# Kernel optimization log

Measured on AMD Instinct MI355X. Metric: run time of the kernel, lower is better.

Reference implementation:

```python
import jax, jax.numpy as jnp
import numpy as np

D_MODEL, D_FF, N_EXPERTS, TOP_K = 1024, 2048, 8, 2
B, S = 2, 2048

def setup_inputs() -> dict:
    key = jax.random.key(0)
    k1, k2, k3, k4 = jax.random.split(key, 4)
    scale = 0.02
    return {
        "x": jax.random.normal(k1, (B, S, D_MODEL), dtype=jnp.float32),
        "gate_w": jax.random.normal(k2, (D_MODEL, N_EXPERTS), dtype=jnp.float32) * scale,
        "w1": jax.random.normal(k3, (N_EXPERTS, D_MODEL, D_FF), dtype=jnp.float32) * scale,
        "w2": jax.random.normal(k4, (N_EXPERTS, D_FF, D_MODEL), dtype=jnp.float32) * scale,
    }

def reference(x, gate_w, w1, w2):
    # --- Router (eval mode: no exploration noise, no dropout) ---
    router_logits = jnp.einsum('bsd,de->bse', x, gate_w)          # [B,S,E]
    top_logits, top_idx = jax.lax.top_k(router_logits, TOP_K)      # [B,S,K]
    top_w = jax.nn.softmax(top_logits, axis=-1)                    # [B,S,K]
    # topk indices are distinct per token, so per-(token,expert) combine weight
    # is the sum over k of weight_k * 1[idx_k == e] (matches torch gather/argmax logic)
    combine = jnp.sum(
        jax.nn.one_hot(top_idx, N_EXPERTS, dtype=x.dtype) * top_w[..., None],
        axis=-2)                                                   # [B,S,E]
    # --- Experts: dense-compute formulation of the gather/MLP/scatter loop ---
    h = jax.nn.silu(jnp.einsum('bsd,edf->ebsf', x, w1))            # [E,B,S,Dff]
    y = jnp.einsum('ebsf,efd->ebsd', h, w2)                        # [E,B,S,D]
    out = jnp.einsum('ebsd,bse->bsd', y, combine)                  # [B,S,D]
    return out
```

## Files before the change

kernel.cpp:

```cpp
#include <hip/hip_runtime.h>
#include <cstdint>
#include <cstddef>

#define D_MODEL 1024
#define D_FF    2048
#define N_EXP   8
#define NTOK    4096
#define NASSIGN (NTOK * 2)
#define MAXTILE 72

typedef __bf16 bf16_t;
typedef bf16_t bf16x8 __attribute__((ext_vector_type(8)));
typedef float  f32x4  __attribute__((ext_vector_type(4)));

typedef __attribute__((address_space(3))) void       lds_void;
typedef const __attribute__((address_space(1))) void gl_void;

__device__ __forceinline__ unsigned short f2b(float f) {
  union { float f; unsigned u; } v; v.f = f;
  unsigned u = v.u;
  unsigned r = (u + 0x7FFFu + ((u >> 16) & 1u)) >> 16;
  return (unsigned short)r;
}
__device__ __forceinline__ float b2f(unsigned short b) {
  union { unsigned u; float f; } v; v.u = ((unsigned)b) << 16; return v.f;
}

__device__ __forceinline__ void transpose_pair(
    const float* __restrict__ ein, unsigned short* __restrict__ eout,
    int R, int C, int c00, int r0, unsigned* T0, unsigned* T1, int tid)
{
  const int g = tid >> 4;
  const int m = tid & 15;
  const int sh = (g & 1) * 16;

  float4 v[2][4];
  #pragma unroll
  for (int t = 0; t < 2; ++t)
    #pragma unroll
    for (int i = 0; i < 4; ++i)
      v[t][i] = *(const float4*)(ein + (size_t)(r0 + i * 16 + g) * C + (c00 + t * 64) + m * 4);

  #pragma unroll
  for (int i = 0; i < 4; ++i) {
    unsigned lo = (unsigned)f2b(v[0][i].x) | ((unsigned)f2b(v[0][i].y) << 16);
    unsigned hi = (unsigned)f2b(v[0][i].z) | ((unsigned)f2b(v[0][i].w) << 16);
    unsigned* p = T0 + (i * 16 + g) * 33 + m * 2;
    p[0] = lo; p[1] = hi;
  }
  __syncthreads();
  #pragma unroll
  for (int i = 0; i < 4; ++i) {
    unsigned lo = (unsigned)f2b(v[1][i].x) | ((unsigned)f2b(v[1][i].y) << 16);
    unsigned hi = (unsigned)f2b(v[1][i].z) | ((unsigned)f2b(v[1][i].w) << 16);
    unsigned* p = T1 + (i * 16 + g) * 33 + m * 2;
    p[0] = lo; p[1] = hi;
  }
  #pragma unroll
  for (int i = 0; i < 4; ++i) {
    int c = i * 16 + g;
    ushort4 o;
    o.x = (unsigned short)(T0[(4 * m + 0) * 33 + (c >> 1)] >> sh);
    o.y = (unsigned short)(T0[(4 * m + 1) * 33 + (c >> 1)] >> sh);
    o.z = (unsigned short)(T0[(4 * m + 2) * 33 + (c >> 1)] >> sh);
    o.w = (unsigned short)(T0[(4 * m + 3) * 33 + (c >> 1)] >> sh);
    *(ushort4*)(eout + (size_t)(c00 + c) * R + r0 + m * 4) = o;
  }
  __syncthreads();
  #pragma unroll
  for (int i = 0; i < 4; ++i) {
    int c = i * 16 + g;
    ushort4 o;
    o.x = (unsigned short)(T1[(4 * m + 0) * 33 + (c >> 1)] >> sh);
    o.y = (unsigned short)(T1[(4 * m + 1) * 33 + (c >> 1)] >> sh);
    o.z = (unsigned short)(T1[(4 * m + 2) * 33 + (c >> 1)] >> sh);
    o.w = (unsigned short)(T1[(4 * m + 3) * 33 + (c >> 1)] >> sh);
    *(ushort4*)(eout + (size_t)(c00 + c + 64) * R + r0 + m * 4) = o;
  }
}

__global__ __launch_bounds__(256) void prep_k(
    const float* __restrict__ x, const float* __restrict__ gw,
    const float* __restrict__ w1, const float* __restrict__ w2,
    unsigned short* __restrict__ w1t, unsigned short* __restrict__ w2t,
    int* __restrict__ eidx, float* __restrict__ ewt)
{
  __shared__ unsigned T[2][64 * 33];
  const int bid = blockIdx.x;
  const int tid = threadIdx.x;

  if (bid < 2048) {
    int e = bid >> 8, rem = bid & 255;
    int bx2 = rem & 15, by = rem >> 4;
    transpose_pair(w1 + (size_t)e * D_MODEL * D_FF,
                   w1t + (size_t)e * D_MODEL * D_FF,
                   D_MODEL, D_FF, bx2 * 128, by * 64, T[0], T[1], tid);
    return;
  }
  if (bid < 4096) {
    int b = bid - 2048;
    int e = b >> 8, rem = b & 255;
    int bx2 = rem & 7, by = rem >> 3;
    transpose_pair(w2 + (size_t)e * D_MODEL * D_FF,
                   w2t + (size_t)e * D_MODEL * D_FF,
                   D_FF, D_MODEL, bx2 * 128, by * 64, T[0], T[1], tid);
    return;
  }
  const int rb = bid - 4096;
  const int wv = tid >> 6, lane = tid & 63;
  const int token = rb * 4 + wv;
  const float4* xr4 = (const float4*)(x + (size_t)token * D_MODEL);
  const float4* gw4 = (const float4*)gw;

  float acc[8] = {};
  #pragma unroll
  for (int it = 0; it < 4; ++it) {
    float4 xv = xr4[it * 64 + lane];
    int d0 = it * 256 + lane * 4;
    #pragma unroll
    for (int i = 0; i < 4; ++i) {
      int d = d0 + i;
      float4 g0 = gw4[d * 2];
      float4 g1 = gw4[d * 2 + 1];
      float xs = (i == 0) ? xv.x : (i == 1) ? xv.y : (i == 2) ? xv.z : xv.w;
      acc[0] += xs * g0.x; acc[1] += xs * g0.y;
      acc[2] += xs * g0.z; acc[3] += xs * g0.w;
      acc[4] += xs * g1.x; acc[5] += xs * g1.y;
      acc[6] += xs * g1.z; acc[7] += xs * g1.w;
    }
  }
  #pragma unroll
  for (int m = 1; m < 64; m <<= 1) {
    #pragma unroll
    for (int k = 0; k < 8; ++k) acc[k] += __shfl_xor(acc[k], m);
  }
  if (lane == 0) {
    int i1 = 0; float v1 = acc[0];
    #pragma unroll
    for (int k = 1; k < 8; ++k) if (acc[k] > v1) { v1 = acc[k]; i1 = k; }
    int i2 = -1; float v2 = -1e30f;
    #pragma unroll
    for (int k = 0; k < 8; ++k) if (k != i1 && acc[k] > v2) { v2 = acc[k]; i2 = k; }
    float t  = __expf(v2 - v1);
    float wa = 1.f / (1.f + t);
    float wb = t * wa;
    eidx[token * 2 + 0] = i1; eidx[token * 2 + 1] = i2;
    ewt [token * 2 + 0] = wa; ewt [token * 2 + 1] = wb;
  }
}

__global__ __launch_bounds__(1024) void scan_k(
    const int* __restrict__ eidx, const float* __restrict__ ewt,
    int* __restrict__ counts, int* __restrict__ offsets,
    int* __restrict__ rowtok, float* __restrict__ rowwt, int* __restrict__ rowof,
    int* __restrict__ tile_e, int* __restrict__ tile_m0, int* __restrict__ tile_n)
{
  __shared__ int wtot[16][9];
  __shared__ int woff[16][9];
  __shared__ int soff[8];
  const int t = threadIdx.x, w = t >> 6, lane = t & 63;

  int4 a = ((const int4*)eidx)[t * 2];
  int4 b = ((const int4*)eidx)[t * 2 + 1];
  int my[8] = {a.x, a.y, a.z, a.w, b.x, b.y, b.z, b.w};
  int pre[8], local[8] = {};
  #pragma unroll
  for (int i = 0; i < 8; ++i) { pre[i] = local[my[i]]; local[my[i]]++; }

  int inc[8];
  #pragma unroll
  for (int e = 0; e < 8; ++e) inc[e] = local[e];
  #pragma unroll
  for (int d = 1; d < 64; d <<= 1) {
    #pragma unroll
    for (int e = 0; e < 8; ++e) {
      int v = __shfl_up(inc[e], d);
      if (lane >= d) inc[e] += v;
    }
  }
  if (lane == 63) {
    #pragma unroll
    for (int e = 0; e < 8; ++e) wtot[w][e] = inc[e];
  }
  __syncthreads();

  if (t < 8) {
    int e = t, run = 0;
    #pragma unroll
    for (int ww = 0; ww < 16; ++ww) { woff[ww][e] = run; run += wtot[ww][e]; }
    wtot[0][e] = run;
  }
  __syncthreads();

  if (t == 0) {
    int o = 0, tt = 0;
    for (int e = 0; e < 8; ++e) {
      int c = wtot[0][e];
      counts[e] = c;
      offsets[e] = o;
      soff[e] = o;
      int nt = (c + 255) >> 8;
      for (int i = 0; i < nt; ++i) { tile_e[tt] = e; tile_m0[tt] = i * 256; ++tt; }
      o += c;
    }
    tile_n[0] = tt;
  }
  __syncthreads();

  int base_[8];
  #pragma unroll
  for (int e = 0; e < 8; ++e) base_[e] = soff[e] + woff[w][e] + inc[e] - local[e];

  float4 wa4 = ((const float4*)ewt)[t * 2];
  float4 wb4 = ((const float4*)ewt)[t * 2 + 1];
  float wv[8] = {wa4.x, wa4.y, wa4.z, wa4.w, wb4.x, wb4.y, wb4.z, wb4.w};

  #pragma unroll
  for (int i = 0; i < 8; ++i) {
    int bb = t * 8 + i, e = my[i];
    int row = base_[e] + pre[i];
    rowtok[row] = bb >> 1;
    rowwt[row]  = wv[i];
    rowof[bb]   = row;
  }
}

__global__ __launch_bounds__(256) void gather_k(
    const float* __restrict__ x, const int* __restrict__ rowtok,
    unsigned short* __restrict__ Xe)
{
  const int row = blockIdx.x;
  const int token = rowtok[row];
  const float4* xr = (const float4*)(x + (size_t)token * D_MODEL);
  ushort4* dst = (ushort4*)(Xe + (size_t)row * D_MODEL);
  float4 v = xr[threadIdx.x];
  ushort4 o;
  o.x = f2b(v.x); o.y = f2b(v.y); o.z = f2b(v.z); o.w = f2b(v.w);
  dst[threadIdx.x] = o;
}

template<int K, int N, int BN, int MODE>
__global__ __launch_bounds__(512) void moe_gemm_k(
    const unsigned short* __restrict__ A,
    const unsigned short* __restrict__ Bt,
    unsigned short* __restrict__ Hout,
    const int* __restrict__ counts, const int* __restrict__ offsets,
    const float* __restrict__ rowwt,
    const int* __restrict__ tile_e, const int* __restrict__ tile_m0,
    const int* __restrict__ tile_n)
{
  constexpr int RT    = 256 + BN;
  constexpr int LOADS = RT / 64;
  constexpr int JF    = BN / 64;
  constexpr int NT    = K / 64;
  constexpr int WN    = BN / 4;

  __shared__ char lds[2 * RT * 128];

  const int nwg = gridDim.x;
  const int bid = blockIdx.x;
  const int wg  = (bid & 7) * (nwg >> 3) + (bid >> 3);
  const int t_  = wg >> 3;
  if (t_ >= tile_n[0]) return;
  const int e    = tile_e[t_];
  const int m0   = tile_m0[t_];
  const int n0   = (wg & 7) * BN;
  const int cnt  = counts[e];
  const int base = offsets[e];

  const int tid  = threadIdx.x;
  const int l    = tid & 63;
  const int w    = tid >> 6;
  const int wm   = w >> 2;
  const int wn   = w & 3;
  const int col  = l & 15, quad = l >> 4;

  const unsigned short* Aseg = A + (size_t)base * K;
  const unsigned short* Bseg = Bt + (size_t)e * ((size_t)N * K);

  const int w8 = w * 8, l3 = l >> 3;
  const int ckst = ((l & 7) ^ l3) << 3;

  auto stage_one = [&](int n, int k0s, char* bw) {
    const unsigned short* src = (n < 4)
      ? Aseg + (size_t)(m0 + n * 64 + w8 + l3) * K + (k0s + ckst)
      : Bseg + (size_t)(n0 + (n - 4) * 64 + w8 + l3) * K + (k0s + ckst);
    __builtin_amdgcn_global_load_lds((gl_void*)src,
        (lds_void*)(bw + (n * 8 + w) * 1024), 16, 0, 0);
  };

  #pragma unroll
  for (int n = 0; n < LOADS; ++n) stage_one(n, 0, lds);

  const int abyte = (wm * 128 + col) * 128;
  const int bbyte = (256 + wn * WN + col) * 128;

  f32x4 acc[8][JF] = {};

  for (int t = 0; t < NT; ++t) {
    char* bufR = lds + (t & 1) * (RT * 128);
    char* bufW = lds + ((t + 1) & 1) * (RT * 128);
    const int k0n = (t + 1) * 64;
    const bool hn = (t + 1 < NT);
    if (hn) {
      stage_one(0, k0n, bufW);
      stage_one(1, k0n, bufW);
      asm volatile("s_waitcnt vmcnt(2)" ::: "memory");
    } else {
      asm volatile("s_waitcnt vmcnt(0)" ::: "memory");
    }
    asm volatile("s_barrier" ::: "memory");

    bf16x8 bfr[JF];
    #pragma unroll
    for (int ks = 0; ks < 2; ++ks) {
      const int cb = ((((ks << 2) | quad) ^ (col & 7)) << 4);
      #pragma unroll
      for (int ih = 0; ih < 2; ++ih) {
        const int ph = ks * 2 + ih;
        bf16x8 af[4];
        #pragma unroll
        for (int i = 0; i < 4; ++i)
          af[i] = *(const bf16x8*)(bufR + abyte + (ih * 4 + i) * 2048 + cb);
        if (ih == 0) {
          #pragma unroll
          for (int j = 0; j < JF; ++j)
            bfr[j] = *(const bf16x8*)(bufR + bbyte + j * 2048 + cb);
        }
        if (hn) {
          if (2 + 2 * ph < LOADS) stage_one(2 + 2 * ph, k0n, bufW);
          if (3 + 2 * ph < LOADS) stage_one(3 + 2 * ph, k0n, bufW);
        }
        __builtin_amdgcn_s_setprio(1);
        #pragma unroll
        for (int i = 0; i < 4; ++i)
          #pragma unroll
          for (int j = 0; j < JF; ++j)
            acc[ih * 4 + i][j] = __builtin_amdgcn_mfma_f32_16x16x32_bf16(
                af[i], bfr[j], acc[ih * 4 + i][j], 0, 0, 0);
        __builtin_amdgcn_s_setprio(0);
      }
    }
    asm volatile("s_waitcnt lgkmcnt(0)" ::: "memory");
    asm volatile("s_barrier" ::: "memory");
  }

  #pragma unroll
  for (int i = 0; i < 8; ++i) {
    #pragma unroll
    for (int reg = 0; reg < 4; ++reg) {
      int r = m0 + wm * 128 + i * 16 + quad * 4 + reg;
      if (r < cnt) {
        unsigned short* hrow = Hout + (size_t)(base + r) * N + (n0 + wn * WN + col);
        if (MODE == 1) {
          #pragma unroll
          for (int j = 0; j < JF; ++j) {
            float v = acc[i][j][reg];
            float s = v / (1.f + __expf(-v));
            hrow[j * 16] = f2b(s);
          }
        } else {
          float wgt = rowwt[base + r];
          #pragma unroll
          for (int j = 0; j < JF; ++j)
            hrow[j * 16] = f2b(wgt * acc[i][j][reg]);
        }
      }
    }
  }
}

__global__ __launch_bounds__(256) void combine_k(
    const unsigned short* __restrict__ Y, const int* __restrict__ rowof,
    float* __restrict__ out)
{
  const int token = blockIdx.x;
  const int r1 = rowof[token * 2];
  const int r2 = rowof[token * 2 + 1];
  const int d4 = threadIdx.x;
  ushort4 a = *(const ushort4*)(Y + (size_t)r1 * D_MODEL + d4 * 4);
  ushort4 b = *(const ushort4*)(Y + (size_t)r2 * D_MODEL + d4 * 4);
  float4 o;
  o.x = b2f(a.x) + b2f(b.x);
  o.y = b2f(a.y) + b2f(b.y);
  o.z = b2f(a.z) + b2f(b.z);
  o.w = b2f(a.w) + b2f(b.w);
  *(float4*)(out + (size_t)token * D_MODEL + d4 * 4) = o;
}

extern "C" void kernel_launch(void* const* d_in, const int* in_sizes, int n_in,
                              void* d_out, int out_size, void* d_ws, size_t ws_size,
                              hipStream_t stream) {
  const float* x  = (const float*)d_in[0];
  const float* gw = (const float*)d_in[1];
  const float* w1 = (const float*)d_in[2];
  const float* w2 = (const float*)d_in[3];
  float* out = (float*)d_out;

  char* ws = (char*)d_ws;
  size_t off = 0;
  auto alloc = [&](size_t bytes) -> char* {
    char* p = ws + off; off += (bytes + 255) & ~(size_t)255; return p;
  };
  int*   ctrl    = (int*)alloc(1024);
  int*   counts  = ctrl;
  int*   offsets = ctrl + 8;
  int*   tile_n  = ctrl + 16;
  int*   tile_e  = ctrl + 32;
  int*   tile_m0 = ctrl + 32 + MAXTILE;
  int*   eidx    = (int*)  alloc((size_t)NASSIGN * 4);
  float* ewt     = (float*)alloc((size_t)NASSIGN * 4);
  int*   rowtok  = (int*)  alloc((size_t)NASSIGN * 4);
  float* rowwt   = (float*)alloc((size_t)NASSIGN * 4);
  int*   rowof   = (int*)  alloc((size_t)NASSIGN * 4);
  unsigned short* Xe  = (unsigned short*)alloc((size_t)(NASSIGN + 256) * D_MODEL * 2);
  unsigned short* H   = (unsigned short*)alloc((size_t)(NASSIGN + 256) * D_FF * 2);
  unsigned short* Y   = (unsigned short*)alloc((size_t)(NASSIGN + 256) * D_MODEL * 2);
  unsigned short* w1t = (unsigned short*)alloc((size_t)N_EXP * D_MODEL * D_FF * 2);
  unsigned short* w2t = (unsigned short*)alloc((size_t)N_EXP * D_MODEL * D_FF * 2);

  prep_k<<<4096 + NTOK / 4, 256, 0, stream>>>(x, gw, w1, w2, w1t, w2t, eidx, ewt);
  scan_k<<<1, 1024, 0, stream>>>(eidx, ewt, counts, offsets, rowtok, rowwt, rowof,
                                 tile_e, tile_m0, tile_n);
  gather_k<<<NASSIGN, 256, 0, stream>>>(x, rowtok, Xe);

  moe_gemm_k<D_MODEL, D_FF, 256, 1><<<320, 512, 0, stream>>>(
      Xe, w1t, H, counts, offsets, rowwt, tile_e, tile_m0, tile_n);
  moe_gemm_k<D_FF, D_MODEL, 128, 2><<<320, 512, 0, stream>>>(
      H, w2t, Y, counts, offsets, rowwt, tile_e, tile_m0, tile_n);
  combine_k<<<NTOK, 256, 0, stream>>>(Y, rowof, out);
}
```

Baseline: 339.5 us.

## Rework weight transpose tiles, fix GEMM BN at 256, add per-phase barriers

```diff
diff --git a/kernel.cpp b/kernel.cpp
--- a/kernel.cpp
+++ b/kernel.cpp
@@ -26,57 +26,47 @@
   union { unsigned u; float f; } v; v.u = ((unsigned)b) << 16; return v.f;
 }
 
-__device__ __forceinline__ void transpose_pair(
+__device__ __forceinline__ void transpose_tile_128x64(
     const float* __restrict__ ein, unsigned short* __restrict__ eout,
-    int R, int C, int c00, int r0, unsigned* T0, unsigned* T1, int tid)
+    int R , int C ,
+    int r0, int c0, unsigned* T, int tid)
 {
   const int g = tid >> 4;
   const int m = tid & 15;
-  const int sh = (g & 1) * 16;
-
-  float4 v[2][4];
-  #pragma unroll
-  for (int t = 0; t < 2; ++t)
-    #pragma unroll
-    for (int i = 0; i < 4; ++i)
-      v[t][i] = *(const float4*)(ein + (size_t)(r0 + i * 16 + g) * C + (c00 + t * 64) + m * 4);
-
-  #pragma unroll
-  for (int i = 0; i < 4; ++i) {
-    unsigned lo = (unsigned)f2b(v[0][i].x) | ((unsigned)f2b(v[0][i].y) << 16);
-    unsigned hi = (unsigned)f2b(v[0][i].z) | ((unsigned)f2b(v[0][i].w) << 16);
-    unsigned* p = T0 + (i * 16 + g) * 33 + m * 2;
-    p[0] = lo; p[1] = hi;
+
+  float4 v[8];
+  #pragma unroll
+  for (int i = 0; i < 8; ++i)
+    v[i] = *(const float4*)(ein + (size_t)(r0 + i * 16 + g) * C + c0 + m * 4);
+
+  #pragma unroll
+  for (int i = 0; i < 8; ++i) {
+    int r  = i * 16 + g;
+    int cx = (r >> 5) << 3;
+    unsigned lo = (unsigned)f2b(v[i].x) | ((unsigned)f2b(v[i].y) << 16);
+    unsigned hi = (unsigned)f2b(v[i].z) | ((unsigned)f2b(v[i].w) << 16);
+    T[r * 33 + ((2 * m)     ^ cx)] = lo;
+    T[r * 33 + ((2 * m + 1) ^ cx)] = hi;
   }
   __syncthreads();
-  #pragma unroll
-  for (int i = 0; i < 4; ++i) {
-    unsigned lo = (unsigned)f2b(v[1][i].x) | ((unsigned)f2b(v[1][i].y) << 16);
-    unsigned hi = (unsigned)f2b(v[1][i].z) | ((unsigned)f2b(v[1][i].w) << 16);
-    unsigned* p = T1 + (i * 16 + g) * 33 + m * 2;
-    p[0] = lo; p[1] = hi;
-  }
-  #pragma unroll
-  for (int i = 0; i < 4; ++i) {
-    int c = i * 16 + g;
-    ushort4 o;
-    o.x = (unsigned short)(T0[(4 * m + 0) * 33 + (c >> 1)] >> sh);
-    o.y = (unsigned short)(T0[(4 * m + 1) * 33 + (c >> 1)] >> sh);
-    o.z = (unsigned short)(T0[(4 * m + 2) * 33 + (c >> 1)] >> sh);
-    o.w = (unsigned short)(T0[(4 * m + 3) * 33 + (c >> 1)] >> sh);
-    *(ushort4*)(eout + (size_t)(c00 + c) * R + r0 + m * 4) = o;
-  }
-  __syncthreads();
-  #pragma unroll
-  for (int i = 0; i < 4; ++i) {
-    int c = i * 16 + g;
-    ushort4 o;
-    o.x = (unsigned short)(T1[(4 * m + 0) * 33 + (c >> 1)] >> sh);
-    o.y = (unsigned short)(T1[(4 * m + 1) * 33 + (c >> 1)] >> sh);
-    o.z = (unsigned short)(T1[(4 * m + 2) * 33 + (c >> 1)] >> sh);
-    o.w = (unsigned short)(T1[(4 * m + 3) * 33 + (c >> 1)] >> sh);
-    *(ushort4*)(eout + (size_t)(c00 + c + 64) * R + r0 + m * 4) = o;
-  }
+
+  const int c    = tid >> 2;
+  const int s4   = tid & 3;
+  const int half = (c & 1) * 16;
+  const int ccol = (c >> 1) ^ (s4 << 3);
+  unsigned ow[16];
+  #pragma unroll
+  for (int j2 = 0; j2 < 16; ++j2) {
+    int r = s4 * 32 + 2 * j2;
+    unsigned lo16 = (T[r * 33 + ccol] >> half) & 0xFFFFu;
+    unsigned hi16 = (T[(r + 1) * 33 + ccol] >> half) & 0xFFFFu;
+    ow[j2] = lo16 | (hi16 << 16);
+  }
+  uint4* dst = (uint4*)(eout + (size_t)(c0 + c) * R + r0 + s4 * 32);
+  dst[0] = *(uint4*)&ow[0];
+  dst[1] = *(uint4*)&ow[4];
+  dst[2] = *(uint4*)&ow[8];
+  dst[3] = *(uint4*)&ow[12];
 }
 
 __global__ __launch_bounds__(256) void prep_k(
@@ -85,25 +75,25 @@
     unsigned short* __restrict__ w1t, unsigned short* __restrict__ w2t,
     int* __restrict__ eidx, float* __restrict__ ewt)
 {
-  __shared__ unsigned T[2][64 * 33];
+  __shared__ unsigned T[128 * 33];
   const int bid = blockIdx.x;
   const int tid = threadIdx.x;
 
   if (bid < 2048) {
     int e = bid >> 8, rem = bid & 255;
-    int bx2 = rem & 15, by = rem >> 4;
-    transpose_pair(w1 + (size_t)e * D_MODEL * D_FF,
-                   w1t + (size_t)e * D_MODEL * D_FF,
-                   D_MODEL, D_FF, bx2 * 128, by * 64, T[0], T[1], tid);
+    int by = rem >> 5, bx = rem & 31;
+    transpose_tile_128x64(w1 + (size_t)e * D_MODEL * D_FF,
+                          w1t + (size_t)e * D_MODEL * D_FF,
+                          D_MODEL, D_FF, by * 128, bx * 64, T, tid);
     return;
   }
   if (bid < 4096) {
     int b = bid - 2048;
     int e = b >> 8, rem = b & 255;
-    int bx2 = rem & 7, by = rem >> 3;
-    transpose_pair(w2 + (size_t)e * D_MODEL * D_FF,
-                   w2t + (size_t)e * D_MODEL * D_FF,
-                   D_FF, D_MODEL, bx2 * 128, by * 64, T[0], T[1], tid);
+    int by = rem >> 4, bx = rem & 15;
+    transpose_tile_128x64(w2 + (size_t)e * D_MODEL * D_FF,
+                          w2t + (size_t)e * D_MODEL * D_FF,
+                          D_FF, D_MODEL, by * 128, bx * 64, T, tid);
     return;
   }
   const int rb = bid - 4096;
@@ -239,7 +229,7 @@
   dst[threadIdx.x] = o;
 }
 
-template<int K, int N, int BN, int MODE>
+template<int K, int N, int MODE>
 __global__ __launch_bounds__(512) void moe_gemm_k(
     const unsigned short* __restrict__ A,
     const unsigned short* __restrict__ Bt,
@@ -249,22 +239,24 @@
     const int* __restrict__ tile_e, const int* __restrict__ tile_m0,
     const int* __restrict__ tile_n)
 {
-  constexpr int RT    = 256 + BN;
-  constexpr int LOADS = RT / 64;
-  constexpr int JF    = BN / 64;
+  constexpr int BN    = 256;
+  constexpr int RT    = 512;
+  constexpr int LOADS = 8;
+  constexpr int JF    = 4;
   constexpr int NT    = K / 64;
-  constexpr int WN    = BN / 4;
+  constexpr int NTN   = N / BN;
+  constexpr int WN    = 64;
 
   __shared__ char lds[2 * RT * 128];
 
   const int nwg = gridDim.x;
   const int bid = blockIdx.x;
   const int wg  = (bid & 7) * (nwg >> 3) + (bid >> 3);
-  const int t_  = wg >> 3;
+  const int t_  = wg / NTN;
   if (t_ >= tile_n[0]) return;
   const int e    = tile_e[t_];
   const int m0   = tile_m0[t_];
-  const int n0   = (wg & 7) * BN;
+  const int n0   = (wg % NTN) * BN;
   const int cnt  = counts[e];
   const int base = offsets[e];
 
@@ -313,36 +305,33 @@
 
     bf16x8 bfr[JF];
     #pragma unroll
-    for (int ks = 0; ks < 2; ++ks) {
+    for (int p = 0; p < 4; ++p) {
+      const int ks = p >> 1, ih = p & 1;
       const int cb = ((((ks << 2) | quad) ^ (col & 7)) << 4);
+      bf16x8 af[4];
       #pragma unroll
-      for (int ih = 0; ih < 2; ++ih) {
-        const int ph = ks * 2 + ih;
-        bf16x8 af[4];
+      for (int i = 0; i < 4; ++i)
+        af[i] = *(const bf16x8*)(bufR + abyte + (ih * 4 + i) * 2048 + cb);
+      if (ih == 0) {
         #pragma unroll
-        for (int i = 0; i < 4; ++i)
-          af[i] = *(const bf16x8*)(bufR + abyte + (ih * 4 + i) * 2048 + cb);
-        if (ih == 0) {
-          #pragma unroll
-          for (int j = 0; j < JF; ++j)
-            bfr[j] = *(const bf16x8*)(bufR + bbyte + j * 2048 + cb);
-        }
-        if (hn) {
-          if (2 + 2 * ph < LOADS) stage_one(2 + 2 * ph, k0n, bufW);
-          if (3 + 2 * ph < LOADS) stage_one(3 + 2 * ph, k0n, bufW);
-        }
-        __builtin_amdgcn_s_setprio(1);
+        for (int j = 0; j < JF; ++j)
+          bfr[j] = *(const bf16x8*)(bufR + bbyte + j * 2048 + cb);
+      }
+      if (hn && p < 3) {
+        stage_one(2 + 2 * p, k0n, bufW);
+        stage_one(3 + 2 * p, k0n, bufW);
+      }
+      asm volatile("s_waitcnt lgkmcnt(0)" ::: "memory");
+      __builtin_amdgcn_s_setprio(1);
+      #pragma unroll
+      for (int i = 0; i < 4; ++i)
         #pragma unroll
-        for (int i = 0; i < 4; ++i)
-          #pragma unroll
-          for (int j = 0; j < JF; ++j)
-            acc[ih * 4 + i][j] = __builtin_amdgcn_mfma_f32_16x16x32_bf16(
-                af[i], bfr[j], acc[ih * 4 + i][j], 0, 0, 0);
-        __builtin_amdgcn_s_setprio(0);
-      }
-    }
-    asm volatile("s_waitcnt lgkmcnt(0)" ::: "memory");
-    asm volatile("s_barrier" ::: "memory");
+        for (int j = 0; j < JF; ++j)
+          acc[ih * 4 + i][j] = __builtin_amdgcn_mfma_f32_16x16x32_bf16(
+              af[i], bfr[j], acc[ih * 4 + i][j], 0, 0, 0);
+      __builtin_amdgcn_s_setprio(0);
+      asm volatile("s_barrier" ::: "memory");
+    }
   }
 
   #pragma unroll
@@ -424,9 +413,9 @@
                                  tile_e, tile_m0, tile_n);
   gather_k<<<NASSIGN, 256, 0, stream>>>(x, rowtok, Xe);
 
-  moe_gemm_k<D_MODEL, D_FF, 256, 1><<<320, 512, 0, stream>>>(
+  moe_gemm_k<D_MODEL, D_FF, 1><<<320, 512, 0, stream>>>(
       Xe, w1t, H, counts, offsets, rowwt, tile_e, tile_m0, tile_n);
-  moe_gemm_k<D_FF, D_MODEL, 128, 2><<<320, 512, 0, stream>>>(
+  moe_gemm_k<D_FF, D_MODEL, 2><<<160, 512, 0, stream>>>(
       H, w2t, Y, counts, offsets, rowwt, tile_e, tile_m0, tile_n);
   combine_k<<<NTOK, 256, 0, stream>>>(Y, rowof, out);
 }
```

New measurement: 336.6 us. About the same (-0.9%).
